# Optimization experiments

Measured on AMD Instinct MI355X. Metric: run time of the kernel, lower is better.

## Reference

```python
import jax, jax.numpy as jnp
import numpy as np

B, S, K, H = 8192, 512, 8, 512  # batch, size_half, n_segments, hidden
EPS = 1e-6


def setup_inputs() -> dict:
    key = jax.random.key(0)
    k0, k1, k2, k3 = jax.random.split(key, 4)
    x_input = jax.random.uniform(k0, (B, 2 * S), dtype=jnp.float32)  # in [0,1)
    log_density = jax.random.normal(k1, (B, 1), dtype=jnp.float32)
    W1 = jax.random.normal(k2, (S, H), dtype=jnp.float32) / np.sqrt(S).astype(np.float32)
    b1 = jnp.zeros((H,), jnp.float32)
    W2 = jax.random.normal(k3, (H, S * (2 * K + 1)), dtype=jnp.float32) / np.sqrt(H).astype(np.float32)
    b2 = jnp.zeros((S * (2 * K + 1),), jnp.float32)
    return {"x_input": x_input, "log_density": log_density,
            "W1": W1, "b1": b1, "W2": W2, "b2": b2}


def reference(x_input, log_density, W1, b1, W2, b2):
    # even_sites=True: passive half a = first S cols, transformed half b = last S
    x_a = x_input[:, :S]
    x_b = x_input[:, S:]

    # NeuralNetwork: Linear -> tanh -> Linear -> tanh (final_activation == activation)
    hid = jnp.tanh((x_a - 0.5) @ W1 + b1)
    net = jnp.tanh(hid @ W2 + b2).reshape(-1, S, 2 * K + 1)  # [B,S,2K+1]
    h_raw, w_raw = net[..., :K + 1], net[..., K + 1:]

    w_norm = jax.nn.softmax(w_raw, axis=2)                       # [B,S,K]
    eh = jnp.exp(h_raw)                                          # [B,S,K+1]
    h_norm = eh / jnp.sum(0.5 * w_norm * (eh[..., :-1] + eh[..., 1:]),
                          axis=2, keepdims=True)

    b = x_a.shape[0]
    x_knots = jnp.concatenate(
        [jnp.full((b, S, 1), -EPS, x_a.dtype), jnp.cumsum(w_norm, axis=2)], axis=2)  # [B,S,K+1]
    pdf_area = 0.5 * w_norm * (h_norm[..., :-1] + h_norm[..., 1:])
    phi_knots = jnp.concatenate(
        [jnp.zeros((b, S, 1), x_a.dtype), jnp.cumsum(pdf_area, axis=2)], axis=2)     # [B,S,K+1]

    # searchsorted(left) - 1 == (# knots strictly below x) - 1
    k_ind = jnp.clip(jnp.sum(x_knots < x_b[..., None], axis=2) - 1, 0, K - 1)[..., None]

    w_k = jnp.take_along_axis(w_norm, k_ind, axis=2)
    h_k = jnp.take_along_axis(h_norm, k_ind, axis=2)
    h_kp1 = jnp.take_along_axis(h_norm, k_ind + 1, axis=2)
    x_km1 = jnp.take_along_axis(x_knots, k_ind, axis=2)
    phi_km1 = jnp.take_along_axis(phi_knots, k_ind, axis=2)

    alpha = (x_b[..., None] - x_km1) / w_k
    phi_b = (phi_km1 + alpha * h_k * w_k
             + 0.5 * alpha ** 2 * (h_kp1 - h_k) * w_k)[..., 0]    # [B,S]

    phi_out = jnp.concatenate([x_a, phi_b], axis=1)               # [B,2S]
    new_log_density = log_density - jnp.sum(
        jnp.log(h_k + alpha * (h_kp1 - h_k)), axis=1)             # [B,1]
    return phi_out, new_log_density
```

## Files before the change

kernel.cpp:

```cpp
#include <hip/hip_runtime.h>
#include <stdint.h>
#include <math.h>

#define BROWS 8192
#define SDIM  512
#define HDIM  512
#define NCOL  8704
#define EPSK  1e-6f
#define LOG2E  1.442695041f
#define TWOL2E 2.885390082f
#define LN2    0.6931471806f

typedef __attribute__((ext_vector_type(8))) short bf16x8;
typedef __attribute__((ext_vector_type(4))) short bf16x4;
typedef __attribute__((ext_vector_type(4))) float f32x4;

__device__ __forceinline__ unsigned short f2bf(float f) {
    unsigned u = __float_as_uint(f);
    u += 0x7fffu + ((u >> 16) & 1u);
    return (unsigned short)(u >> 16);
}
__device__ __forceinline__ unsigned short f2bf_fast(float f) {
    return (unsigned short)((__float_as_uint(f) + 0x8000u) >> 16);
}
__device__ __forceinline__ float bf2f(unsigned short s) {
    return __uint_as_float(((unsigned)s) << 16);
}
#define EXP2F(x) __builtin_amdgcn_exp2f(x)
#define LOG2F(x) __builtin_amdgcn_logf(x)
#define RCPF(x)  __builtin_amdgcn_rcpf(x)

__device__ __forceinline__ float ftanh(float x) {
    float e = EXP2F(TWOL2E * x);
    return (e - 1.f) * RCPF(e + 1.f);
}
__device__ __forceinline__ float ftanh_l2e(float acc, float bias2L) {
    float e = EXP2F(fmaf(acc, TWOL2E, bias2L));
    return fmaf(e, LOG2E, -LOG2E) * RCPF(e + 1.f);
}

#define GLD16(g, l)                                                         \
    __builtin_amdgcn_global_load_lds(                                       \
        (const __attribute__((address_space(1))) void*)(g),                 \
        (__attribute__((address_space(3))) void*)(l), 16, 0, 0)

__global__ __launch_bounds__(256) void prep_k(
    const float* __restrict__ W2, unsigned short* __restrict__ W2p,
    const float* __restrict__ W1, unsigned short* __restrict__ W1T,
    const float* __restrict__ logd, float* __restrict__ out)
{
    __shared__ float tile[32 * 33];
    const int t = threadIdx.x;
    if (blockIdx.x < 544) {
        const int ct = blockIdx.x;
        const int colbase = ct * 16;
        const int colblk = ct / 17;
        const int chunk  = ct - colblk * 17;
        const int k32 = t >> 3;
        const int c2  = (t & 7) * 2;
        const int r   = t >> 4;
        const int e2  = (t & 15) * 2;
        for (int kk = 0; kk < 16; ++kk) {
            float2 v = *(const float2*)&W2[(size_t)(kk * 32 + k32) * NCOL + colbase + c2];
            __syncthreads();
            tile[k32 * 17 + c2 + 0] = v.x;
            tile[k32 * 17 + c2 + 1] = v.y;
            __syncthreads();
            const size_t off = (((size_t)colblk * 16 + kk) * 17 + chunk) * 512;
            ushort2 o;
            o.x = f2bf(tile[(e2 + 0) * 17 + r]);
            o.y = f2bf(tile[(e2 + 1) * 17 + r]);
            *(ushort2*)&W2p[off + (size_t)r * 32 + e2] = o;
        }
    } else if (blockIdx.x < 800) {
        const int bt = blockIdx.x - 544;
        const int cb = (bt & 15) * 32;
        const int rb = (bt >> 4) * 32;
        const int ty = t >> 3, tx = (t & 7) * 4;
        float4 v = *(const float4*)&W1[(size_t)(rb + ty) * HDIM + cb + tx];
        tile[ty * 33 + tx + 0] = v.x;
        tile[ty * 33 + tx + 1] = v.y;
        tile[ty * 33 + tx + 2] = v.z;
        tile[ty * 33 + tx + 3] = v.w;
        __syncthreads();
        const int oy = t >> 3, ox = (t & 7) * 4;
        bf16x4 o;
        o[0] = (short)f2bf(tile[(ox + 0) * 33 + oy]);
        o[1] = (short)f2bf(tile[(ox + 1) * 33 + oy]);
        o[2] = (short)f2bf(tile[(ox + 2) * 33 + oy]);
        o[3] = (short)f2bf(tile[(ox + 3) * 33 + oy]);
        *(bf16x4*)&W1T[(size_t)(cb + oy) * SDIM + rb + ox] = o;
    } else {
        const int b = (blockIdx.x - 800) * 256 + t;
        out[(size_t)BROWS * (2 * SDIM) + b] = logd[b];
    }
}

__global__ __launch_bounds__(256) void gemm1_mfma(
    const float* __restrict__ x,
    const unsigned short* __restrict__ W1T,
    const float* __restrict__ b1,
    unsigned short* __restrict__ hid,
    float* __restrict__ out)
{
    __shared__ short As[64 * 32];
    __shared__ short Bs[128 * 32];
    const int bm   = blockIdx.y * 64;
    const int bn   = blockIdx.x * 128;
    const int tid  = threadIdx.x;
    const int lane = tid & 63;
    const int wave = tid >> 6;
    const int ln15 = lane & 15;
    const int quad = lane >> 4;
    const int wm   = (wave >> 1) * 32;
    const int wn   = (wave & 1) * 64;
    const int arow = tid >> 2, aseg = tid & 3;
    const int brow = lane >> 2, bsub = lane & 3;

    f32x4 acc[2][4];
#pragma unroll
    for (int i = 0; i < 2; i++)
#pragma unroll
        for (int j = 0; j < 4; j++) acc[i][j] = (f32x4){0.f, 0.f, 0.f, 0.f};

    for (int k0 = 0; k0 < SDIM; k0 += 32) {
        const float4* xq = (const float4*)&x[(size_t)(bm + arow) * (2 * SDIM) + k0 + aseg * 8];
        float4 f0 = xq[0], f1 = xq[1];
        if (blockIdx.x == 0) {
            float* op = &out[(size_t)(bm + arow) * (2 * SDIM) + k0 + aseg * 8];
            *(float4*)op = f0;
            *(float4*)(op + 4) = f1;
        }
        __syncthreads();
#pragma unroll
        for (int c = 0; c < 2; c++) {
            const int chunk = wave * 2 + c;
            GLD16(&W1T[(size_t)(bn + chunk * 16 + brow) * SDIM + k0 + bsub * 8],
                  &Bs[chunk * 512]);
        }
        bf16x8 v0;
        v0[0] = (short)f2bf_fast(f0.x - 0.5f); v0[1] = (short)f2bf_fast(f0.y - 0.5f);
        v0[2] = (short)f2bf_fast(f0.z - 0.5f); v0[3] = (short)f2bf_fast(f0.w - 0.5f);
        v0[4] = (short)f2bf_fast(f1.x - 0.5f); v0[5] = (short)f2bf_fast(f1.y - 0.5f);
        v0[6] = (short)f2bf_fast(f1.z - 0.5f); v0[7] = (short)f2bf_fast(f1.w - 0.5f);
        *(bf16x8*)&As[arow * 32 + aseg * 8] = v0;
        __syncthreads();

        bf16x8 af[2], bfr[4];
#pragma unroll
        for (int i = 0; i < 2; i++)
            af[i] = *(const bf16x8*)&As[(wm + i * 16 + ln15) * 32 + quad * 8];
#pragma unroll
        for (int j = 0; j < 4; j++)
            bfr[j] = *(const bf16x8*)&Bs[(wn + j * 16 + ln15) * 32 + quad * 8];
#pragma unroll
        for (int i = 0; i < 2; i++)
#pragma unroll
            for (int j = 0; j < 4; j++)
                acc[i][j] = __builtin_amdgcn_mfma_f32_16x16x32_bf16(af[i], bfr[j], acc[i][j], 0, 0, 0);
    }

#pragma unroll
    for (int j = 0; j < 4; j++) {
        const int col = bn + wn + j * 16 + ln15;
        const float bias = b1[col];
#pragma unroll
        for (int i = 0; i < 2; i++) {
#pragma unroll
            for (int r = 0; r < 4; r++) {
                const int row = bm + wm + i * 16 + quad * 4 + r;
                hid[(size_t)row * HDIM + col] = f2bf(ftanh(acc[i][j][r] + bias));
            }
        }
    }
}

__global__ __launch_bounds__(256, 3) void gemm2_spline_mfma(
    const unsigned short* __restrict__ hid,
    const unsigned short* __restrict__ W2p,
    const float* __restrict__ b2,
    const float* __restrict__ x,
    float* __restrict__ out)
{
    __shared__ short smem[2 * 10752];

    const int bm   = blockIdx.y * 64;
    const int tid  = threadIdx.x;
    const int lane = tid & 63;
    const int wave = tid >> 6;
    const int ln15 = lane & 15;
    const int quad = lane >> 4;
    const int brow = lane >> 2, bsub = lane & 3;
    const int jstart = wave * 4;
    const int jcount = (wave == 3) ? 5 : 4;
    const int bcol = blockIdx.x * 272;

    f32x4 acc[4][5];
#pragma unroll
    for (int i = 0; i < 4; i++)
#pragma unroll
        for (int j = 0; j < 5; j++) acc[i][j] = (f32x4){0.f, 0.f, 0.f, 0.f};

    const unsigned short* bbase =
        W2p + ((size_t)blockIdx.x * 16) * 17 * 512 + (size_t)lane * 8;
    const unsigned short* abase =
        &hid[(size_t)(bm + wave * 16 + brow) * HDIM + bsub * 8];

    auto issue = [&](int n, int p) {
        short* dst = smem + p * 10752;
        GLD16(abase + n * 32, &dst[wave * 512]);
        const unsigned short* bk = bbase + (size_t)n * (17 * 512);
        for (int c = 0; c < jcount; ++c) {
            const int chunk = jstart + c;
            GLD16(bk + (size_t)chunk * 512, &dst[2048 + chunk * 512]);
        }
    };

    issue(0, 0);
    for (int n = 0; n < 16; ++n) {
        __syncthreads();
        if (n < 15) issue(n + 1, (n + 1) & 1);
        const short* As = smem + (n & 1) * 10752;
        const short* Bs = As + 2048;

        bf16x8 af[4];
#pragma unroll
        for (int i = 0; i < 4; i++)
            af[i] = *(const bf16x8*)&As[(i * 16 + ln15) * 32 + quad * 8];

#define KSTEP(JC)                                                               \
        _Pragma("unroll") for (int j = 0; j < (JC); ++j) {                      \
            bf16x8 bfr = *(const bf16x8*)&Bs[((jstart + j) * 16 + ln15) * 32 + quad * 8]; \
            _Pragma("unroll") for (int i = 0; i < 4; ++i)                       \
                acc[i][j] = __builtin_amdgcn_mfma_f32_16x16x32_bf16(af[i], bfr, acc[i][j], 0, 0, 0); \
        }
        if (wave == 3) { KSTEP(5) } else { KSTEP(4) }
#undef KSTEP
    }

    const int sp = tid & 15;
    const int r0 = tid >> 4;
    const int sglob = blockIdx.x * 16 + sp;
    float xbv[4];
#pragma unroll
    for (int t = 0; t < 4; ++t)
        xbv[t] = x[(size_t)(bm + t * 16 + r0) * (2 * SDIM) + SDIM + sglob];

    __syncthreads();
#define EPI1(JC)                                                                \
    _Pragma("unroll") for (int j = 0; j < (JC); ++j) {                          \
        const int col_l = (jstart + j) * 16 + ln15;                             \
        const int spc   = (col_l * 241) >> 12;         \
        const int cc    = col_l - spc * 17;                                     \
        const int basej = spc * 20 + cc;                                        \
        const float bias2L = b2[bcol + col_l] * TWOL2E;                         \
        _Pragma("unroll") for (int i = 0; i < 4; ++i)                           \
            _Pragma("unroll") for (int r = 0; r < 4; ++r) {                     \
                const int row_l = i * 16 + quad * 4 + r;                        \
                smem[row_l * 328 + basej] =                                     \
                    (short)f2bf_fast(ftanh_l2e(acc[i][j][r], bias2L));          \
            }                                                                   \
    }
    if (wave == 3) { EPI1(5) } else { EPI1(4) }
#undef EPI1
    __syncthreads();

    for (int t = 0; t < 4; ++t) {
        const int row_l = t * 16 + r0;
        const int row = bm + row_l;
        const int base2 = row_l * 328 + sp * 20;
        bf16x4 a0 = *(const bf16x4*)&smem[base2 + 0];
        bf16x4 a1 = *(const bf16x4*)&smem[base2 + 4];
        bf16x4 a2 = *(const bf16x4*)&smem[base2 + 8];
        bf16x4 a3 = *(const bf16x4*)&smem[base2 + 12];
        const short p2 = smem[base2 + 16];

        float s[17];
#pragma unroll
        for (int c = 0; c < 4; c++) {
            s[c]      = bf2f((unsigned short)a0[c]);
            s[4 + c]  = bf2f((unsigned short)a1[c]);
            s[8 + c]  = bf2f((unsigned short)a2[c]);
            s[12 + c] = bf2f((unsigned short)a3[c]);
        }
        s[16] = bf2f((unsigned short)p2);

        float eh[9], e[8];
#pragma unroll
        for (int j = 0; j < 9; j++) eh[j] = EXP2F(s[j]);
#pragma unroll
        for (int c = 0; c < 8; c++) e[c]  = EXP2F(s[9 + c]);

        float cum_e[8], cum_u[8];
        cum_e[0] = e[0];
        cum_u[0] = e[0] * (eh[0] + eh[1]);
#pragma unroll
        for (int c = 1; c < 8; c++) {
            cum_e[c] = cum_e[c - 1] + e[c];
            cum_u[c] = fmaf(e[c], eh[c] + eh[c + 1], cum_u[c - 1]);
        }
        const float se = cum_e[7];
        const float su = cum_u[7];
        const float thr = xbv[t] * se;

        float selE = e[0], selEH = eh[0], selEH1 = eh[1];
        float selCE = -EPSK * se, selCU = 0.f;
#pragma unroll
        for (int c = 1; c < 8; c++) {
            const bool tt = (cum_e[c - 1] < thr);
            selE   = tt ? e[c]         : selE;
            selEH  = tt ? eh[c]        : selEH;
            selEH1 = tt ? eh[c + 1]    : selEH1;
            selCE  = tt ? cum_e[c - 1] : selCE;
            selCU  = tt ? cum_u[c - 1] : selCU;
        }

        const float alpha = (thr - selCE) * RCPF(selE);
        const float dlt   = selEH1 - selEH;
        const float su_inv = RCPF(su);
        float p = fmaf(2.f * alpha, selE * selEH, selCU);
        p = fmaf(alpha * alpha, selE * dlt, p);
        out[(size_t)row * (2 * SDIM) + SDIM + sglob] = p * su_inv;

        const float g = fmaf(alpha, dlt, selEH) * (2.f * se * su_inv);
        float lg = LOG2F(g);
        lg += __shfl_xor(lg, 1);
        lg += __shfl_xor(lg, 2);
        lg += __shfl_xor(lg, 4);
        lg += __shfl_xor(lg, 8);
        if (sp == 0)
            atomicAdd(&out[(size_t)BROWS * (2 * SDIM) + row], -lg * LN2);
    }
}

extern "C" void kernel_launch(void* const* d_in, const int* in_sizes, int n_in,
                              void* d_out, int out_size, void* d_ws, size_t ws_size,
                              hipStream_t stream) {
    const float* x    = (const float*)d_in[0];
    const float* logd = (const float*)d_in[1];
    const float* W1   = (const float*)d_in[2];
    const float* b1   = (const float*)d_in[3];
    const float* W2   = (const float*)d_in[4];
    const float* b2   = (const float*)d_in[5];
    float* out = (float*)d_out;

    char* ws = (char*)d_ws;
    unsigned short* W1T = (unsigned short*)(ws + 32768);
    unsigned short* W2p = (unsigned short*)(ws + 557056);
    unsigned short* hid = (unsigned short*)(ws + 9469952);

    prep_k<<<832, 256, 0, stream>>>(W2, W2p, W1, W1T, logd, out);
    gemm1_mfma<<<dim3(4, 128), 256, 0, stream>>>(x, W1T, b1, hid, out);
    gemm2_spline_mfma<<<dim3(32, 128), 256, 0, stream>>>(hid, W2p, b2, x, out);
}
```

Before: 244.7 us.

## Swap gemm2 grid axes and store epilogue tile column-major in LDS

```diff
diff --git a/kernel.cpp b/kernel.cpp
--- a/kernel.cpp
+++ b/kernel.cpp
@@ -184,7 +184,8 @@
 {
     __shared__ short smem[2 * 10752];
 
-    const int bm   = blockIdx.y * 64;
+    const int bm     = blockIdx.x * 64;
+    const int colblk = blockIdx.y;
     const int tid  = threadIdx.x;
     const int lane = tid & 63;
     const int wave = tid >> 6;
@@ -193,7 +194,7 @@
     const int brow = lane >> 2, bsub = lane & 3;
     const int jstart = wave * 4;
     const int jcount = (wave == 3) ? 5 : 4;
-    const int bcol = blockIdx.x * 272;
+    const int bcol = colblk * 272;
 
     f32x4 acc[4][5];
 #pragma unroll
@@ -202,7 +203,7 @@
         for (int j = 0; j < 5; j++) acc[i][j] = (f32x4){0.f, 0.f, 0.f, 0.f};
 
     const unsigned short* bbase =
-        W2p + ((size_t)blockIdx.x * 16) * 17 * 512 + (size_t)lane * 8;
+        W2p + ((size_t)colblk * 16) * 17 * 512 + (size_t)lane * 8;
     const unsigned short* abase =
         &hid[(size_t)(bm + wave * 16 + brow) * HDIM + bsub * 8];
 
@@ -240,7 +241,7 @@
 
     const int sp = tid & 15;
     const int r0 = tid >> 4;
-    const int sglob = blockIdx.x * 16 + sp;
+    const int sglob = colblk * 16 + sp;
     float xbv[4];
 #pragma unroll
     for (int t = 0; t < 4; ++t)
@@ -250,16 +251,13 @@
 #define EPI1(JC)                                                                \
     _Pragma("unroll") for (int j = 0; j < (JC); ++j) {                          \
         const int col_l = (jstart + j) * 16 + ln15;                             \
-        const int spc   = (col_l * 241) >> 12;         \
-        const int cc    = col_l - spc * 17;                                     \
-        const int basej = spc * 20 + cc;                                        \
         const float bias2L = b2[bcol + col_l] * TWOL2E;                         \
-        _Pragma("unroll") for (int i = 0; i < 4; ++i)                           \
-            _Pragma("unroll") for (int r = 0; r < 4; ++r) {                     \
-                const int row_l = i * 16 + quad * 4 + r;                        \
-                smem[row_l * 328 + basej] =                                     \
-                    (short)f2bf_fast(ftanh_l2e(acc[i][j][r], bias2L));          \
-            }                                                                   \
+        _Pragma("unroll") for (int i = 0; i < 4; ++i) {                         \
+            bf16x4 o;                                                           \
+            _Pragma("unroll") for (int r = 0; r < 4; ++r)                       \
+                o[r] = (short)f2bf_fast(ftanh_l2e(acc[i][j][r], bias2L));       \
+            *(bf16x4*)&smem[col_l * 68 + i * 16 + quad * 4] = o;                \
+        }                                                                       \
     }
     if (wave == 3) { EPI1(5) } else { EPI1(4) }
 #undef EPI1
@@ -268,22 +266,12 @@
     for (int t = 0; t < 4; ++t) {
         const int row_l = t * 16 + r0;
         const int row = bm + row_l;
-        const int base2 = row_l * 328 + sp * 20;
-        bf16x4 a0 = *(const bf16x4*)&smem[base2 + 0];
-        bf16x4 a1 = *(const bf16x4*)&smem[base2 + 4];
-        bf16x4 a2 = *(const bf16x4*)&smem[base2 + 8];
-        bf16x4 a3 = *(const bf16x4*)&smem[base2 + 12];
-        const short p2 = smem[base2 + 16];
+        const int cbase = sp * 17 * 68 + row_l;
 
         float s[17];
 #pragma unroll
-        for (int c = 0; c < 4; c++) {
-            s[c]      = bf2f((unsigned short)a0[c]);
-            s[4 + c]  = bf2f((unsigned short)a1[c]);
-            s[8 + c]  = bf2f((unsigned short)a2[c]);
-            s[12 + c] = bf2f((unsigned short)a3[c]);
-        }
-        s[16] = bf2f((unsigned short)p2);
+        for (int c = 0; c < 17; c++)
+            s[c] = bf2f((unsigned short)smem[cbase + c * 68]);
 
         float eh[9], e[8];
 #pragma unroll
@@ -351,5 +339,5 @@
 
     prep_k<<<832, 256, 0, stream>>>(W2, W2p, W1, W1T, logd, out);
     gemm1_mfma<<<dim3(4, 128), 256, 0, stream>>>(x, W1T, b1, hid, out);
-    gemm2_spline_mfma<<<dim3(32, 128), 256, 0, stream>>>(hid, W2p, b2, x, out);
-}
+    gemm2_spline_mfma<<<dim3(128, 32), 256, 0, stream>>>(hid, W2p, b2, x, out);
+}
```

Result: no change. 241.1 us (-1.4%).
